# Kernel tuning notes

Hardware: AMD Instinct MI355X
Metric: run time of the kernel (lower is better)

## Reference

```python
import jax, jax.numpy as jnp
import numpy as np

EPS = 1e-5
NUM_HEADS = 16


def activation_quant(x):
    # 8-bit activation quant with straight-through estimator
    scale = 127.0 / jnp.clip(jnp.max(jnp.abs(x), axis=-1, keepdims=True), 1e-5, None)
    y = jnp.clip(jnp.round(x * scale), -128.0, 127.0) / scale
    return x + jax.lax.stop_gradient(y - x)


def weight_quant(w):
    # ternary {-1,0,1} weight quant with STE
    scale = 1.0 / jnp.clip(jnp.mean(jnp.abs(w)), 1e-5, None)
    wq = jnp.clip(jnp.round(w * scale), -1.0, 1.0) / scale
    return w + jax.lax.stop_gradient(wq - w)


def bitlinear(x, w):
    # F.layer_norm(x, x.shape[1:]): normalize over ALL dims except batch, no affine
    axes = tuple(range(1, x.ndim))
    mu = jnp.mean(x, axis=axes, keepdims=True)
    var = jnp.var(x, axis=axes, keepdims=True)
    xn = (x - mu) * jax.lax.rsqrt(var + EPS)
    return jnp.einsum('bnd,od->bno', activation_quant(xn), weight_quant(w))


def layer_norm(x, gamma, beta):
    mu = jnp.mean(x, axis=-1, keepdims=True)
    var = jnp.var(x, axis=-1, keepdims=True)
    return (x - mu) * jax.lax.rsqrt(var + EPS) * gamma + beta


def setup_inputs() -> dict:
    key = jax.random.key(0)
    k0, k1, k2 = jax.random.split(key, 3)
    B, N, D = 2, 2048, 1024
    return {
        't': jnp.zeros((1,), jnp.float32),
        'x': jax.random.normal(k0, (B, N, D), jnp.float32),
        'w_qkv': jax.random.normal(k1, (3 * D, D), jnp.float32) * 0.02,
        'w_out': jax.random.normal(k2, (D, D), jnp.float32) * 0.02,
        'gamma': jnp.ones((D,), jnp.float32),
        'beta': jnp.zeros((D,), jnp.float32),
    }


def reference(t, x, w_qkv, w_out, gamma, beta):
    B, N, D = x.shape
    H = NUM_HEADS
    hd = D // H
    scale = hd ** -0.5
    h = layer_norm(x, gamma, beta)                     # [B,N,D]
    qkv = bitlinear(h, w_qkv).reshape(B, N, 3, H, hd)   # [B,N,3,H,hd]
    qkv = jnp.transpose(qkv, (2, 0, 3, 1, 4))           # [3,B,H,N,hd]
    q, k, v = qkv[0], qkv[1], qkv[2]
    attn = jax.nn.softmax(jnp.einsum('bhnd,bhmd->bhnm', q, k) * scale, axis=-1)
    out = jnp.einsum('bhnm,bhmd->bhnd', attn, v)        # [B,H,N,hd]
    out = jnp.transpose(out, (0, 2, 1, 3)).reshape(B, N, D)
    return bitlinear(out, w_out)
```

## Files before the change

### kernel.cpp

```cpp
#include <hip/hip_runtime.h>
#include <hip/hip_bf16.h>
#include <hip/hip_fp16.h>
#include <math.h>

typedef __hip_bfloat16 bf16;
typedef int   i32x4  __attribute__((ext_vector_type(4)));
typedef float f32x4  __attribute__((ext_vector_type(4)));
typedef float f32x16 __attribute__((ext_vector_type(16)));
typedef short bfx8   __attribute__((ext_vector_type(8)));

#define EPSV 1e-5f
#define NROWS 4096
#define DIM   1024
#define NSEQ  2048

__device__ __forceinline__ float fexp2(float x){ return __builtin_amdgcn_exp2f(x); }

__device__ __forceinline__ float ldv(const void* p, size_t i, int dt){
  if (dt == 0) return ((const float*)p)[i];
  if (dt == 1) return __bfloat162float(((const bf16*)p)[i]);
  return __half2float(((const __half*)p)[i]);
}
__device__ __forceinline__ float b2f(unsigned u){
  return __uint_as_float(u << 16);
}
__device__ __forceinline__ unsigned short f2bu(float f){
  bf16 t = __float2bfloat16(f);
  return *reinterpret_cast<unsigned short*>(&t);
}

__device__ __forceinline__ void detect(const void* c0, const void* c1,
                                       int& dt, const void*& g, const void*& bta){
  unsigned u0 = *(const unsigned*)c0;
  int gfirst = (u0 != 0u) ? 1 : 0;
  g   = gfirst ? c0 : c1;
  bta = gfirst ? c1 : c0;
  unsigned short g0 = *(const unsigned short*)g;
  dt = (g0 == 0x3F80) ? 1 : ((g0 == 0x3C00) ? 2 : 0);
}

__device__ __forceinline__ float blk_sum(float v, float* sm){
  #pragma unroll
  for (int o = 32; o > 0; o >>= 1) v += __shfl_xor(v, o, 64);
  __syncthreads();
  if ((threadIdx.x & 63) == 0) sm[threadIdx.x >> 6] = v;
  __syncthreads();
  return sm[0] + sm[1] + sm[2] + sm[3];
}
__device__ __forceinline__ double blk_sum_d(double v, double* sm){
  #pragma unroll
  for (int o = 32; o > 0; o >>= 1) v += __shfl_xor(v, o, 64);
  __syncthreads();
  if ((threadIdx.x & 63) == 0) sm[threadIdx.x >> 6] = v;
  __syncthreads();
  return sm[0] + sm[1] + sm[2] + sm[3];
}
__device__ __forceinline__ float blk_max(float v, float* sm){
  #pragma unroll
  for (int o = 32; o > 0; o >>= 1) v = fmaxf(v, __shfl_xor(v, o, 64));
  __syncthreads();
  if ((threadIdx.x & 63) == 0) sm[threadIdx.x >> 6] = v;
  __syncthreads();
  return fmaxf(fmaxf(sm[0], sm[1]), fmaxf(sm[2], sm[3]));
}

__global__ __launch_bounds__(256) void ln_abs(const void* __restrict__ x,
                                              const void* __restrict__ c0,
                                              const void* __restrict__ c1,
                                              const void* __restrict__ wq,
                                              const void* __restrict__ wo,
                                              unsigned short* __restrict__ h,
                                              double* __restrict__ lnp,
                                              double* __restrict__ awp1,
                                              double* __restrict__ awp2){
  __shared__ float sm[4];
  __shared__ double smd[4];
  int dt; const void *g, *bta;
  detect(c0, c1, dt, g, bta);
  int tid = threadIdx.x;
  if (blockIdx.x < 4096){
    int row = blockIdx.x;
    float v[4]; float s = 0.f;
    float gmv[4], btv[4];
    if (dt == 0){
      float4 v4 = ((const float4*)x)[(size_t)row*256 + tid];
      v[0]=v4.x; v[1]=v4.y; v[2]=v4.z; v[3]=v4.w;
      float4 gm4 = ((const float4*)g)[tid];
      float4 bt4 = ((const float4*)bta)[tid];
      gmv[0]=gm4.x; gmv[1]=gm4.y; gmv[2]=gm4.z; gmv[3]=gm4.w;
      btv[0]=bt4.x; btv[1]=bt4.y; btv[2]=bt4.z; btv[3]=bt4.w;
    } else {
      size_t base = (size_t)row * DIM;
      #pragma unroll
      for (int i = 0; i < 4; ++i){
        v[i]   = ldv(x, base + 4*tid + i, dt);
        gmv[i] = ldv(g, 4*tid + i, dt);
        btv[i] = ldv(bta, 4*tid + i, dt);
      }
    }
    #pragma unroll
    for (int i = 0; i < 4; ++i) s += v[i];
    s = blk_sum(s, sm);
    float mu = s * (1.f/1024.f);
    float d2 = 0.f;
    #pragma unroll
    for (int i = 0; i < 4; ++i){ float d = v[i] - mu; d2 += d*d; }
    d2 = blk_sum(d2, sm);
    float rs = rsqrtf(d2 * (1.f/1024.f) + EPSV);
    float hv[4];
    #pragma unroll
    for (int i = 0; i < 4; ++i) hv[i] = (v[i]-mu)*rs*gmv[i] + btv[i];
    unsigned p0 = (unsigned)f2bu(hv[0]) | ((unsigned)f2bu(hv[1]) << 16);
    unsigned p1 = (unsigned)f2bu(hv[2]) | ((unsigned)f2bu(hv[3]) << 16);
    ((uint2*)h)[(size_t)row*256 + tid] = make_uint2(p0, p1);
    double hs = 0.0, hq = 0.0;
    #pragma unroll
    for (int i = 0; i < 4; ++i){ hs += (double)hv[i]; hq += (double)hv[i]*(double)hv[i]; }
    hs = blk_sum_d(hs, smd);
    hq = blk_sum_d(hq, smd);
    if (tid == 0){ lnp[2*row] = hs; lnp[2*row + 1] = hq; }
  } else {
    int blk = blockIdx.x - 4096;
    const void* w; int n; int nblk; int bi; double* part;
    if (blk < 512){ w = wq; n = 3*DIM*DIM; nblk = 512; bi = blk;      part = awp1; }
    else          { w = wo; n = DIM*DIM;   nblk = 128; bi = blk - 512; part = awp2; }
    double s = 0.0;
    if (dt == 0){
      const float4* w4 = (const float4*)w;
      int n4 = n >> 2;
      for (int i = bi*256 + tid; i < n4; i += nblk*256){
        float4 v = w4[i];
        s += (double)(fabsf(v.x) + fabsf(v.y)) + (double)(fabsf(v.z) + fabsf(v.w));
      }
    } else {
      for (int i = bi*256 + tid; i < n; i += nblk*256)
        s += (double)fabsf(ldv(w, i, dt));
    }
    s = blk_sum_d(s, smd);
    if (tid == 0) part[bi] = s;
  }
}

__global__ __launch_bounds__(256) void finalize1(float* acc,
                                                 const double* __restrict__ lnp,
                                                 const double* __restrict__ awp1,
                                                 const double* __restrict__ awp2){
  __shared__ double smd[4];
  int tid = threadIdx.x;
  double s0=0, q0=0, s1=0, q1=0, a1=0, a2=0;
  for (int i = tid; i < 2048; i += 256){
    s0 += lnp[2*i];          q0 += lnp[2*i + 1];
    s1 += lnp[2*(i+2048)];   q1 += lnp[2*(i+2048) + 1];
  }
  for (int i = tid; i < 512; i += 256) a1 += awp1[i];
  if (tid < 128) a2 = awp2[tid];
  s0 = blk_sum_d(s0, smd);  q0 = blk_sum_d(q0, smd);
  s1 = blk_sum_d(s1, smd);  q1 = blk_sum_d(q1, smd);
  a1 = blk_sum_d(a1, smd);  a2 = blk_sum_d(a2, smd);
  if (tid == 0){
    const double cnt = 2097152.0;
    double mu0 = s0/cnt, var0 = q0/cnt - mu0*mu0;
    double mu1 = s1/cnt, var1 = q1/cnt - mu1*mu1;
    acc[16] = (float)mu0; acc[17] = (float)(1.0 / sqrt(var0 + 1e-5));
    acc[18] = (float)mu1; acc[19] = (float)(1.0 / sqrt(var1 + 1e-5));
    acc[20] = (float)(1.0 / fmax(a1 / (3.0*1024.0*1024.0), 1e-5));
    acc[21] = (float)(1.0 / fmax(a2 / (1024.0*1024.0), 1e-5));
  }
}

__global__ __launch_bounds__(256) void finalize2(float* acc,
                                                 const double* __restrict__ atp){
  __shared__ double smd[4];
  int tid = threadIdx.x;
  double s0=0, q0=0, s1=0, q1=0;
  for (int i = tid; i < 1024; i += 256){
    s0 += atp[2*i];           q0 += atp[2*i + 1];
    s1 += atp[2*(i+1024)];    q1 += atp[2*(i+1024) + 1];
  }
  s0 = blk_sum_d(s0, smd);  q0 = blk_sum_d(q0, smd);
  s1 = blk_sum_d(s1, smd);  q1 = blk_sum_d(q1, smd);
  if (tid == 0){
    const double cnt = 2097152.0;
    double mu0 = s0/cnt, var0 = q0/cnt - mu0*mu0;
    double mu1 = s1/cnt, var1 = q1/cnt - mu1*mu1;
    acc[22] = (float)mu0; acc[23] = (float)(1.0 / sqrt(var0 + 1e-5));
    acc[24] = (float)mu1; acc[25] = (float)(1.0 / sqrt(var1 + 1e-5));
  }
}

__global__ __launch_bounds__(256) void quant1_w(const unsigned short* __restrict__ buf,
                                                signed char* __restrict__ qout,
                                                float* __restrict__ rscale,
                                                const void* __restrict__ wqv,
                                                const void* __restrict__ wov,
                                                signed char* __restrict__ wqk,
                                                signed char* __restrict__ wqo,
                                                const float* __restrict__ acc,
                                                const void* __restrict__ c0,
                                                const void* __restrict__ c1){
  __shared__ float sm[4];
  int tid = threadIdx.x;
  if (blockIdx.x < 4096){
    int row = blockIdx.x;
    int b = row >> 11;
    float mu = acc[16 + 2*b], rs = acc[17 + 2*b];
    uint2 pk2 = ((const uint2*)buf)[(size_t)row*256 + tid];
    float v[4];
    v[0] = (b2f(pk2.x & 0xffffu) - mu) * rs;
    v[1] = (b2f(pk2.x >> 16)     - mu) * rs;
    v[2] = (b2f(pk2.y & 0xffffu) - mu) * rs;
    v[3] = (b2f(pk2.y >> 16)     - mu) * rs;
    float am = fmaxf(fmaxf(fabsf(v[0]), fabsf(v[1])), fmaxf(fabsf(v[2]), fabsf(v[3])));
    am = blk_max(am, sm);
    am = fmaxf(am, 1e-5f);
    float s127 = 127.f / am;
    unsigned pk = 0;
    #pragma unroll
    for (int i = 0; i < 4; ++i){
      float q = rintf(v[i] * s127);
      q = fminf(fmaxf(q, -128.f), 127.f);
      pk |= ((unsigned)(unsigned char)(signed char)q) << (8*i);
    }
    ((unsigned*)qout)[(size_t)row*256 + tid] = pk;
    if (tid == 0) rscale[row] = am * (1.f/127.f);
  } else {
    int dt; const void *g, *bta;
    detect(c0, c1, dt, g, bta);
    int bi = blockIdx.x - 4096;
    const int NQ4 = 786432;
    const int NT4 = 1048576;
    float s1 = acc[20], s2 = acc[21];
    if (dt == 0){
      for (int i = bi*256 + tid; i < NT4; i += 1024*256){
        int inq = (i < NQ4);
        const float4* src = inq ? (const float4*)wqv : (const float4*)wov;
        unsigned* dst = inq ? (unsigned*)wqk : (unsigned*)wqo;
        int idx = inq ? i : (i - NQ4);
        float scale = inq ? s1 : s2;
        float4 v = src[idx];
        float vv[4] = {v.x, v.y, v.z, v.w};
        unsigned pk = 0;
        #pragma unroll
        for (int j = 0; j < 4; ++j){
          float q = rintf(vv[j] * scale);
          q = fminf(fmaxf(q, -1.f), 1.f);
          pk |= ((unsigned)(unsigned char)(signed char)q) << (8*j);
        }
        dst[idx] = pk;
      }
    } else {
      const int NQ = 3*DIM*DIM, NT = 4*DIM*DIM;
      for (int i = bi*256 + tid; i < NT; i += 1024*256){
        int inq = (i < NQ);
        int idx = inq ? i : (i - NQ);
        float scale = inq ? s1 : s2;
        float q = rintf(ldv(inq ? wqv : wov, idx, dt) * scale);
        q = fminf(fmaxf(q, -1.f), 1.f);
        (inq ? wqk : wqo)[idx] = (signed char)q;
      }
    }
  }
}

__global__ __launch_bounds__(256) void act_quant_i8b(const unsigned short* __restrict__ buf,
                                                     signed char* __restrict__ qout,
                                                     float* __restrict__ rscale,
                                                     const float* __restrict__ acc,
                                                     int statOff){
  __shared__ float sm[4];
  int row = blockIdx.x;
  int b = row >> 11;
  float mu = acc[statOff + 2*b], rs = acc[statOff + 2*b + 1];
  int tid = threadIdx.x;
  uint2 pk2 = ((const uint2*)buf)[(size_t)row*256 + tid];
  float v[4];
  v[0] = (b2f(pk2.x & 0xffffu) - mu) * rs;
  v[1] = (b2f(pk2.x >> 16)     - mu) * rs;
  v[2] = (b2f(pk2.y & 0xffffu) - mu) * rs;
  v[3] = (b2f(pk2.y >> 16)     - mu) * rs;
  float am = fmaxf(fmaxf(fabsf(v[0]), fabsf(v[1])), fmaxf(fabsf(v[2]), fabsf(v[3])));
  am = blk_max(am, sm);
  am = fmaxf(am, 1e-5f);
  float s127 = 127.f / am;
  unsigned pk = 0;
  #pragma unroll
  for (int i = 0; i < 4; ++i){
    float q = rintf(v[i] * s127);
    q = fminf(fmaxf(q, -128.f), 127.f);
    pk |= ((unsigned)(unsigned char)(signed char)q) << (8*i);
  }
  ((unsigned*)qout)[(size_t)row*256 + tid] = pk;
  if (tid == 0) rscale[row] = am * (1.f/127.f);
}

__global__ __launch_bounds__(256) void gemm_i8(const signed char* __restrict__ A,
                                               const signed char* __restrict__ W,
                                               const float* __restrict__ rscale,
                                               const float* __restrict__ acc, int sidx,
                                               float* __restrict__ Cf,
                                               bf16* __restrict__ Cb,
                                               int ldc, int writeBf, float q_prescale){
  __shared__ __attribute__((aligned(16))) signed char Asl[128][80];
  __shared__ __attribute__((aligned(16))) signed char Bsl[128][80];
  int tid = threadIdx.x, lane = tid & 63, w = tid >> 6;
  int wr = w >> 1, wc = w & 1;

  int nwgx = gridDim.x;
  int flat = blockIdx.y * nwgx + blockIdx.x;
  int nwg  = nwgx * gridDim.y;
  int cpx  = nwg >> 3;
  int swz  = (flat & 7) * cpx + (flat >> 3);
  int r0 = (swz / nwgx) * 128, o0 = (swz % nwgx) * 128;

  i32x4 zz = {0,0,0,0};
  i32x4 accv[4][4];
  #pragma unroll
  for (int m = 0; m < 4; ++m)
    #pragma unroll
    for (int n = 0; n < 4; ++n) accv[m][n] = zz;

  int sr0 = tid >> 2, sr1 = sr0 + 64;
  int sc  = (tid & 3) * 16;

  i32x4 a0, a1, b0, b1;
  a0 = *(const i32x4*)(A + (size_t)(r0 + sr0)*1024 + sc);
  a1 = *(const i32x4*)(A + (size_t)(r0 + sr1)*1024 + sc);
  b0 = *(const i32x4*)(W + (size_t)(o0 + sr0)*1024 + sc);
  b1 = *(const i32x4*)(W + (size_t)(o0 + sr1)*1024 + sc);

  for (int k0 = 0; k0 < 1024; k0 += 64){
    __syncthreads();
    *(i32x4*)&Asl[sr0][sc] = a0;
    *(i32x4*)&Asl[sr1][sc] = a1;
    *(i32x4*)&Bsl[sr0][sc] = b0;
    *(i32x4*)&Bsl[sr1][sc] = b1;
    __syncthreads();
    if (k0 + 64 < 1024){
      int kn = k0 + 64;
      a0 = *(const i32x4*)(A + (size_t)(r0 + sr0)*1024 + kn + sc);
      a1 = *(const i32x4*)(A + (size_t)(r0 + sr1)*1024 + kn + sc);
      b0 = *(const i32x4*)(W + (size_t)(o0 + sr0)*1024 + kn + sc);
      b1 = *(const i32x4*)(W + (size_t)(o0 + sr1)*1024 + kn + sc);
    }
    i32x4 af[4], bfr[4];
    #pragma unroll
    for (int m = 0; m < 4; ++m)
      af[m] = *(const i32x4*)&Asl[wr*64 + m*16 + (lane & 15)][(lane >> 4) * 16];
    #pragma unroll
    for (int n = 0; n < 4; ++n)
      bfr[n] = *(const i32x4*)&Bsl[wc*64 + n*16 + (lane & 15)][(lane >> 4) * 16];
    __builtin_amdgcn_s_setprio(1);
    #pragma unroll
    for (int m = 0; m < 4; ++m)
      #pragma unroll
      for (int n = 0; n < 4; ++n)
        accv[m][n] = __builtin_amdgcn_mfma_i32_16x16x64_i8(af[m], bfr[n], accv[m][n], 0, 0, 0);
    __builtin_amdgcn_s_setprio(0);
  }

  float wsc = acc[sidx];
  float cs = (o0 < 1024) ? q_prescale : 1.0f;
  float rf[4][4];
  #pragma unroll
  for (int m = 0; m < 4; ++m)
    #pragma unroll
    for (int r = 0; r < 4; ++r)
      rf[m][r] = rscale[r0 + wr*64 + m*16 + ((lane >> 4) << 2) + r] / wsc * cs;

  #pragma unroll
  for (int m = 0; m < 4; ++m)
    #pragma unroll
    for (int n = 0; n < 4; ++n)
      #pragma unroll
      for (int r = 0; r < 4; ++r){
        float val = (float)accv[m][n][r] * rf[m][r];
        size_t row = (size_t)(r0 + wr*64 + m*16 + ((lane >> 4) << 2) + r);
        int col = o0 + wc*64 + n*16 + (lane & 15);
        if (writeBf) Cb[row * ldc + col] = __float2bfloat16(val);
        else         Cf[row * ldc + col] = val;
      }
}

__global__ __launch_bounds__(128) void attn_mfma(const bf16* __restrict__ qkv,
                                                 unsigned short* __restrict__ out,
                                                 double* __restrict__ atp){
  __shared__ __attribute__((aligned(16))) unsigned short K_lds[2][64][64];
  __shared__ __attribute__((aligned(16))) unsigned short Vt_lds[2][64][64];

  int tid = threadIdx.x, lane = tid & 63, w = tid >> 6;
  int l31 = lane & 31, hi = lane >> 5;

  int flat = blockIdx.y * 32 + blockIdx.x;
  int slot = flat & 7, idx = flat >> 3;
  int bh = slot * 4 + (idx >> 5);
  int qx = idx & 31;
  int b = bh >> 4, h = bh & 15;
  int n0 = qx * 64;
  const unsigned short* qg = (const unsigned short*)qkv;

  char* kB = (char*)K_lds;
  char* vB = (char*)Vt_lds;

  int qrow = b*NSEQ + n0 + w*32 + l31;
  bfx8 qf[4];
  #pragma unroll
  for (int kk = 0; kk < 4; ++kk)
    qf[kk] = *(const bfx8*)(qg + (size_t)qrow*3072 + h*64 + kk*16 + hi*8);

  float m_run = -INFINITY, l_run = 0.f;
  f32x16 acco[2];
  #pragma unroll
  for (int n = 0; n < 2; ++n)
    #pragma unroll
    for (int r = 0; r < 16; ++r) acco[n][r] = 0.f;

  int krow = tid & 63;
  int r2 = tid & 31, dw = tid >> 5;
  int k7 = krow & 7;
  int q7 = l31 & 7;

  bfx8 kc[4], vv[4];
  auto LOADT = [&](int kt){
    size_t kvb = (size_t)(b*NSEQ + kt*64);
    #pragma unroll
    for (int j = 0; j < 4; ++j)
      kc[j] = *(const bfx8*)(qg + (kvb + krow)*3072 + 1024 + h*64 + (w + 2*j)*8);
    vv[0] = *(const bfx8*)(qg + (kvb + 2*r2    )*3072 + 2048 + h*64 + dw*8);
    vv[1] = *(const bfx8*)(qg + (kvb + 2*r2 + 1)*3072 + 2048 + h*64 + dw*8);
    vv[2] = *(const bfx8*)(qg + (kvb + 2*r2    )*3072 + 2048 + h*64 + (dw+4)*8);
    vv[3] = *(const bfx8*)(qg + (kvb + 2*r2 + 1)*3072 + 2048 + h*64 + (dw+4)*8);
  };
  auto WRITET = [&](int buf){
    int bo = buf * 8192;
    #pragma unroll
    for (int j = 0; j < 4; ++j)
      *(bfx8*)(kB + bo + krow*128 + (((w + 2*j) ^ k7) << 4)) = kc[j];
    #pragma unroll
    for (int u = 0; u < 8; ++u){
      unsigned w0 = (unsigned)(unsigned short)vv[0][u] |
                    ((unsigned)(unsigned short)vv[1][u] << 16);
      unsigned w1 = (unsigned)(unsigned short)vv[2][u] |
                    ((unsigned)(unsigned short)vv[3][u] << 16);
      *(unsigned*)(vB + bo + (dw*8 + u)*128     + ((4*r2) ^ (u << 4))) = w0;
      *(unsigned*)(vB + bo + ((dw+4)*8 + u)*128 + ((4*r2) ^ (u << 4))) = w1;
    }
  };

  LOADT(0);
  WRITET(0);
  __syncthreads();
  LOADT(1);

  int cur = 0;
  for (int kt = 0; kt < NSEQ/64; ++kt){
    if (kt + 1 < NSEQ/64){
      WRITET(cur ^ 1);
      if (kt + 2 < NSEQ/64) LOADT(kt + 2);
    }
    int bo = cur * 8192;

    f32x16 s0, s1;
    #pragma unroll
    for (int r = 0; r < 16; ++r){ s0[r] = 0.f; s1[r] = 0.f; }
    #pragma unroll
    for (int kk = 0; kk < 4; ++kk){
      bfx8 kb0 = *(const bfx8*)(kB + bo + l31*128        + (((2*kk + hi) ^ q7) << 4));
      bfx8 kb1 = *(const bfx8*)(kB + bo + (32 + l31)*128 + (((2*kk + hi) ^ q7) << 4));
      __builtin_amdgcn_s_setprio(1);
      s0 = __builtin_amdgcn_mfma_f32_32x32x16_bf16(kb0, qf[kk], s0, 0, 0, 0);
      s1 = __builtin_amdgcn_mfma_f32_32x32x16_bf16(kb1, qf[kk], s1, 0, 0, 0);
      __builtin_amdgcn_s_setprio(0);
    }

    float pa0 = fmaxf(s0[0], s0[1]),  pa1 = fmaxf(s0[2], s0[3]);
    float pa2 = fmaxf(s0[4], s0[5]),  pa3 = fmaxf(s0[6], s0[7]);
    #pragma unroll
    for (int r = 8; r < 16; r += 4){
      pa0 = fmaxf(pa0, fmaxf(s0[r], s0[r+1]));
      pa1 = fmaxf(pa1, fmaxf(s0[r+2], s0[r+3]));
    }
    #pragma unroll
    for (int r = 0; r < 16; r += 4){
      pa2 = fmaxf(pa2, fmaxf(s1[r], s1[r+1]));
      pa3 = fmaxf(pa3, fmaxf(s1[r+2], s1[r+3]));
    }
    float pm = fmaxf(fmaxf(pa0, pa1), fmaxf(pa2, pa3));
    pm = fmaxf(pm, __shfl_xor(pm, 32, 64));
    if (__any(pm > m_run + 11.5415605f)){
      float mnew = fmaxf(m_run, pm);
      float corr = fexp2(m_run - mnew);
      m_run = mnew;
      l_run *= corr;
      #pragma unroll
      for (int r = 0; r < 16; ++r){
        float ca = __shfl(corr, (r & 3) + 8*(r >> 2) + 4*hi, 64);
        acco[0][r] *= ca; acco[1][r] *= ca;
      }
    }
    float ts = 0.f;
    #pragma unroll
    for (int r = 0; r < 16; ++r){
      s0[r] = fexp2(s0[r] - m_run); ts += s0[r];
      s1[r] = fexp2(s1[r] - m_run); ts += s1[r];
    }
    ts += __shfl_xor(ts, 32, 64);
    l_run += ts;

    #pragma unroll
    for (int kvb2 = 0; kvb2 < 2; ++kvb2){
      const f32x16& s = kvb2 ? s1 : s0;
      #pragma unroll
      for (int kk2 = 0; kk2 < 2; ++kk2){
        int bse = kk2 * 8;
        unsigned wa, wb2, wc, wd;
        asm("v_cvt_pk_bf16_f32 %0, %1, %2" : "=v"(wa)  : "v"(s[bse+0]), "v"(s[bse+1]));
        asm("v_cvt_pk_bf16_f32 %0, %1, %2" : "=v"(wb2) : "v"(s[bse+4]), "v"(s[bse+5]));
        asm("v_cvt_pk_bf16_f32 %0, %1, %2" : "=v"(wc)  : "v"(s[bse+2]), "v"(s[bse+3]));
        asm("v_cvt_pk_bf16_f32 %0, %1, %2" : "=v"(wd)  : "v"(s[bse+6]), "v"(s[bse+7]));
        asm("v_permlane32_swap_b32 %0, %1" : "+v"(wa), "+v"(wb2));
        asm("v_permlane32_swap_b32 %0, %1" : "+v"(wc), "+v"(wd));
        unsigned pw[4] = {wa, wc, wb2, wd};
        bfx8 pfr = *(bfx8*)pw;
        #pragma unroll
        for (int n = 0; n < 2; ++n){
          bfx8 vb = *(const bfx8*)(vB + bo + (n*32 + l31)*128 +
                                   (((kvb2*4 + kk2*2 + hi) ^ q7) << 4));
          __builtin_amdgcn_s_setprio(1);
          acco[n] = __builtin_amdgcn_mfma_f32_32x32x16_bf16(pfr, vb, acco[n], 0, 0, 0);
          __builtin_amdgcn_s_setprio(0);
        }
      }
    }

    __syncthreads();
    cur ^= 1;
  }

  float il = 1.f / l_run;
  float ila[16];
  #pragma unroll
  for (int r = 0; r < 16; ++r)
    ila[r] = __shfl(il, (r & 3) + 8*(r >> 2) + 4*hi, 64);
  double ssum = 0.0, ssq = 0.0;
  #pragma unroll
  for (int n = 0; n < 2; ++n)
    #pragma unroll
    for (int r = 0; r < 16; ++r){
      float o = acco[n][r] * ila[r];
      int orow = b*NSEQ + n0 + w*32 + (r & 3) + 8*(r >> 2) + 4*hi;
      out[(size_t)orow * DIM + h*64 + n*32 + l31] = f2bu(o);
      ssum += (double)o; ssq += (double)o * (double)o;
    }
  #pragma unroll
  for (int o2 = 32; o2 > 0; o2 >>= 1){
    ssum += __shfl_xor(ssum, o2, 64);
    ssq  += __shfl_xor(ssq,  o2, 64);
  }
  if (lane == 0){
    int widx = (bh * 32 + qx) * 2 + w;
    atp[2*widx] = ssum; atp[2*widx + 1] = ssq;
  }
}

extern "C" void kernel_launch(void* const* d_in, const int* in_sizes, int n_in,
                              void* d_out, int out_size, void* d_ws, size_t ws_size,
                              hipStream_t stream) {
  int ix = -1, iwq = -1, iwo = -1, ig0 = -1, ig1 = -1;
  for (int i = 0; i < n_in; ++i){
    int s = in_sizes[i];
    if      (s == 4194304) ix  = i;
    else if (s == 3145728) iwq = i;
    else if (s == 1048576) iwo = i;
    else if (s == 1024){ if (ig0 < 0) ig0 = i; else ig1 = i; }
  }
  if (ix < 0 || iwq < 0 || iwo < 0 || ig0 < 0 || ig1 < 0){ ix=1; iwq=2; iwo=3; ig0=4; ig1=5; }
  const void* x     = d_in[ix];
  const void* w_qkv = d_in[iwq];
  const void* w_out = d_in[iwo];
  const void* g0    = d_in[ig0];
  const void* g1    = d_in[ig1];

  char* ws = (char*)d_ws;
  float*  acc     = (float*)ws;
  float*  rscale1 = (float*)(ws + 12288);
  float*  rscale2 = (float*)(ws + 28672);
  double* lnp     = (double*)(ws + 65536);
  double* awp1    = (double*)(ws + 131072);
  double* awp2    = (double*)(ws + 135168);
  double* atp     = (double*)(ws + 139264);
  unsigned short* h    = (unsigned short*)(ws + (1u<<20));
  signed char*  h_i8   = (signed char*)(ws + (17u<<20));
  signed char*  wqk_i8 = (signed char*)(ws + (21u<<20));
  signed char*  wqo_i8 = (signed char*)(ws + (24u<<20));
  bf16*         qkvb   = (bf16*)       (ws + (25u<<20));
  signed char*  a2_i8  = (signed char*)(ws + (49u<<20));
  unsigned short* aout = h;

  ln_abs<<<4736, 256, 0, stream>>>(x, g0, g1, w_qkv, w_out, h, lnp, awp1, awp2);
  finalize1<<<1, 256, 0, stream>>>(acc, lnp, awp1, awp2);
  quant1_w<<<5120, 256, 0, stream>>>(h, h_i8, rscale1, w_qkv, w_out,
                                     wqk_i8, wqo_i8, acc, g0, g1);
  gemm_i8<<<dim3(24, 32), 256, 0, stream>>>(h_i8, wqk_i8, rscale1, acc, 20,
                                            nullptr, qkvb, 3072, 1, 0.125f * 1.44269504f);
  attn_mfma<<<dim3(32, 32), 128, 0, stream>>>(qkvb, aout, atp);
  finalize2<<<1, 256, 0, stream>>>(acc, atp);
  act_quant_i8b<<<NROWS, 256, 0, stream>>>(aout, a2_i8, rscale2, acc, 22);
  gemm_i8<<<dim3(8, 32), 256, 0, stream>>>(a2_i8, wqo_i8, rscale2, acc, 21,
                                           (float*)d_out, nullptr, 1024, 0, 1.0f);
}
```

Before: 147.3 us.

## Double-buffer int8 GEMM tiles via direct global-to-LDS loads with XOR swizzle

The int8 GEMM now fetches A and W tiles with global_load_lds straight into a double-buffered LDS tile, so the register staging and the extra LDS store step go away. The next k-tile's load is issued before the current tile's MFMAs, leaving one barrier per iteration instead of two. Padded rows are replaced by an XOR swizzle on 16-byte chunks to avoid LDS bank conflicts. The risk is correctness of the wave-wide LDS destination layout and the lack of an explicit vmcnt wait before the barrier.

```diff
diff --git a/kernel.cpp b/kernel.cpp
--- a/kernel.cpp
+++ b/kernel.cpp
@@ -13,6 +13,10 @@
 #define NROWS 4096
 #define DIM   1024
 #define NSEQ  2048
+
+#define GLDS(gp, lp) __builtin_amdgcn_global_load_lds( \
+    (const __attribute__((address_space(1))) void*)(gp), \
+    (__attribute__((address_space(3))) void*)(lp), 16, 0, 0)
 
 __device__ __forceinline__ float fexp2(float x){ return __builtin_amdgcn_exp2f(x); }
 
@@ -300,17 +304,18 @@
                                                float* __restrict__ Cf,
                                                bf16* __restrict__ Cb,
                                                int ldc, int writeBf, float q_prescale){
-  __shared__ __attribute__((aligned(16))) signed char Asl[128][80];
-  __shared__ __attribute__((aligned(16))) signed char Bsl[128][80];
+  __shared__ __attribute__((aligned(16))) signed char Asl[2][128][64];
+  __shared__ __attribute__((aligned(16))) signed char Bsl[2][128][64];
   int tid = threadIdx.x, lane = tid & 63, w = tid >> 6;
   int wr = w >> 1, wc = w & 1;
+  int l15 = lane & 15, g = lane >> 4;
 
   int nwgx = gridDim.x;
   int flat = blockIdx.y * nwgx + blockIdx.x;
   int nwg  = nwgx * gridDim.y;
   int cpx  = nwg >> 3;
-  int swz  = (flat & 7) * cpx + (flat >> 3);
-  int r0 = (swz / nwgx) * 128, o0 = (swz % nwgx) * 128;
+  int swzb = (flat & 7) * cpx + (flat >> 3);
+  int r0 = (swzb / nwgx) * 128, o0 = (swzb % nwgx) * 128;
 
   i32x4 zz = {0,0,0,0};
   i32x4 accv[4][4];
@@ -319,36 +324,37 @@
     #pragma unroll
     for (int n = 0; n < 4; ++n) accv[m][n] = zz;
 
-  int sr0 = tid >> 2, sr1 = sr0 + 64;
-  int sc  = (tid & 3) * 16;
-
-  i32x4 a0, a1, b0, b1;
-  a0 = *(const i32x4*)(A + (size_t)(r0 + sr0)*1024 + sc);
-  a1 = *(const i32x4*)(A + (size_t)(r0 + sr1)*1024 + sc);
-  b0 = *(const i32x4*)(W + (size_t)(o0 + sr0)*1024 + sc);
-  b1 = *(const i32x4*)(W + (size_t)(o0 + sr1)*1024 + sc);
-
+  int srow = (w << 4) | (lane >> 2);
+  int sws  = ((lane >> 2) ^ (lane >> 4)) & 3;
+  int srcb = (((lane & 3) ^ sws) << 4);
+  const signed char* gA0 = A + (size_t)(r0 + srow)*1024 + srcb;
+  const signed char* gA1 = A + (size_t)(r0 + srow + 64)*1024 + srcb;
+  const signed char* gB0 = W + (size_t)(o0 + srow)*1024 + srcb;
+  const signed char* gB1 = W + (size_t)(o0 + srow + 64)*1024 + srcb;
+
+  auto GLOADT = [&](int buf, int kq){
+    GLDS(gA0 + kq, &Asl[buf][w*16][0]);
+    GLDS(gA1 + kq, &Asl[buf][w*16 + 64][0]);
+    GLDS(gB0 + kq, &Bsl[buf][w*16][0]);
+    GLDS(gB1 + kq, &Bsl[buf][w*16 + 64][0]);
+  };
+
+  GLOADT(0, 0);
+  __syncthreads();
+
+  int swr = (l15 ^ (l15 >> 2)) & 3;
+  int cb  = ((g ^ swr) << 4);
+
+  int cur = 0;
   for (int k0 = 0; k0 < 1024; k0 += 64){
-    __syncthreads();
-    *(i32x4*)&Asl[sr0][sc] = a0;
-    *(i32x4*)&Asl[sr1][sc] = a1;
-    *(i32x4*)&Bsl[sr0][sc] = b0;
-    *(i32x4*)&Bsl[sr1][sc] = b1;
-    __syncthreads();
-    if (k0 + 64 < 1024){
-      int kn = k0 + 64;
-      a0 = *(const i32x4*)(A + (size_t)(r0 + sr0)*1024 + kn + sc);
-      a1 = *(const i32x4*)(A + (size_t)(r0 + sr1)*1024 + kn + sc);
-      b0 = *(const i32x4*)(W + (size_t)(o0 + sr0)*1024 + kn + sc);
-      b1 = *(const i32x4*)(W + (size_t)(o0 + sr1)*1024 + kn + sc);
-    }
+    if (k0 + 64 < 1024) GLOADT(cur ^ 1, k0 + 64);
     i32x4 af[4], bfr[4];
     #pragma unroll
     for (int m = 0; m < 4; ++m)
-      af[m] = *(const i32x4*)&Asl[wr*64 + m*16 + (lane & 15)][(lane >> 4) * 16];
+      af[m] = *(const i32x4*)&Asl[cur][wr*64 + m*16 + l15][cb];
     #pragma unroll
     for (int n = 0; n < 4; ++n)
-      bfr[n] = *(const i32x4*)&Bsl[wc*64 + n*16 + (lane & 15)][(lane >> 4) * 16];
+      bfr[n] = *(const i32x4*)&Bsl[cur][wc*64 + n*16 + l15][cb];
     __builtin_amdgcn_s_setprio(1);
     #pragma unroll
     for (int m = 0; m < 4; ++m)
@@ -356,6 +362,8 @@
       for (int n = 0; n < 4; ++n)
         accv[m][n] = __builtin_amdgcn_mfma_i32_16x16x64_i8(af[m], bfr[n], accv[m][n], 0, 0, 0);
     __builtin_amdgcn_s_setprio(0);
+    __syncthreads();
+    cur ^= 1;
   }
 
   float wsc = acc[sidx];
@@ -375,7 +383,7 @@
       for (int r = 0; r < 4; ++r){
         float val = (float)accv[m][n][r] * rf[m][r];
         size_t row = (size_t)(r0 + wr*64 + m*16 + ((lane >> 4) << 2) + r);
-        int col = o0 + wc*64 + n*16 + (lane & 15);
+        int col = o0 + wc*64 + n*16 + l15;
         if (writeBf) Cb[row * ldc + col] = __float2bfloat16(val);
         else         Cf[row * ldc + col] = val;
       }
```

Result: no change. 147.7 us (median of 3 runs) (+0.3%).
